# Optimization experiments

Measured on AMD Instinct MI355X. Metric: run time of the kernel, lower is better.

## Reference

```python
import jax, jax.numpy as jnp
import numpy as np

B, T, D = 1, 2048, 1024
H = 16
HD = D // H
K = 4
FF = 4 * D
LAYERS = 24
EPS = 1.1920929e-07  # torch.finfo(float32).eps, RMSNorm default


def setup_inputs() -> dict:
    key = jax.random.key(0)
    ks = jax.random.split(key, 16)
    s = 0.02
    return {
        "x": jax.random.normal(ks[0], (B, T, D), jnp.float32),
        "gamma": jax.random.uniform(ks[1], (D,), jnp.float32),
        "beta": jax.random.normal(ks[2], (D,), jnp.float32) * 0.1,
        "iter_scale": jax.random.uniform(ks[3], (1,), jnp.float32),
        "qkv_bases": jax.random.normal(ks[4], (K, 3 * D, D), jnp.float32) * s,
        "o_bases": jax.random.normal(ks[5], (K, D, D), jnp.float32) * s,
        "gate_bases": jax.random.normal(ks[6], (K, FF, D), jnp.float32) * s,
        "up_bases": jax.random.normal(ks[7], (K, FF, D), jnp.float32) * s,
        "down_bases": jax.random.normal(ks[8], (K, D, FF), jnp.float32) * s,
        "alpha_qkv": jax.random.normal(ks[9], (LAYERS, K), jnp.float32) * 0.1 + jnp.eye(LAYERS, K)[:, :K] * 0.0 + jnp.concatenate([jnp.ones((LAYERS, 1)), jnp.zeros((LAYERS, K - 1))], axis=1),
        "alpha_o": jnp.concatenate([jnp.ones((LAYERS, 1)), jnp.zeros((LAYERS, K - 1))], axis=1) + jax.random.normal(ks[10], (LAYERS, K)) * 0.1,
        "alpha_gate": jnp.concatenate([jnp.ones((LAYERS, 1)), jnp.zeros((LAYERS, K - 1))], axis=1) + jax.random.normal(ks[11], (LAYERS, K)) * 0.1,
        "alpha_up": jnp.concatenate([jnp.ones((LAYERS, 1)), jnp.zeros((LAYERS, K - 1))], axis=1) + jax.random.normal(ks[12], (LAYERS, K)) * 0.1,
        "alpha_down": jnp.concatenate([jnp.ones((LAYERS, 1)), jnp.zeros((LAYERS, K - 1))], axis=1) + jax.random.normal(ks[13], (LAYERS, K)) * 0.1,
        "norm1_w": jnp.ones((D,), jnp.float32),
        "norm2_w": jnp.ones((D,), jnp.float32),
        "layer_idx": 5,
    }


def _rmsnorm(x, w):
    return x * jax.lax.rsqrt(jnp.mean(x * x, axis=-1, keepdims=True) + EPS) * w


def reference(x, gamma, beta, iter_scale, qkv_bases, o_bases, gate_bases, up_bases,
              down_bases, alpha_qkv, alpha_o, alpha_gate, alpha_up, alpha_down,
              norm1_w, norm2_w, layer_idx):
    Bx, Tx, Dx = x.shape
    # --- attention sub-block ---
    h = _rmsnorm(x, norm1_w) * gamma + beta
    W_qkv = jnp.einsum('k,kij->ij', alpha_qkv[layer_idx], qkv_bases)  # [3D, D]
    qkv = jnp.einsum('btd,od->bto', h, W_qkv).reshape(Bx, Tx, 3, H, HD)
    qkv = jnp.transpose(qkv, (2, 0, 3, 1, 4))  # [3, B, H, T, HD]
    q, k, v = qkv[0], qkv[1], qkv[2]
    scores = jnp.einsum('bhqd,bhkd->bhqk', q, k) / jnp.sqrt(jnp.asarray(HD, x.dtype))
    causal = jnp.tril(jnp.ones((Tx, Tx), bool))
    scores = jnp.where(causal, scores, jnp.asarray(-jnp.inf, scores.dtype))
    attn = jax.nn.softmax(scores, axis=-1)
    out = jnp.einsum('bhqk,bhkd->bhqd', attn, v)
    out = jnp.transpose(out, (0, 2, 1, 3)).reshape(Bx, Tx, Dx)
    W_o = jnp.einsum('k,kij->ij', alpha_o[layer_idx], o_bases)
    x_attn = x + jnp.einsum('btd,od->bto', out, W_o)
    # --- SwiGLU FFN sub-block ---
    h2 = _rmsnorm(x_attn, norm2_w) * gamma + beta
    W_g = jnp.einsum('k,kij->ij', alpha_gate[layer_idx], gate_bases)
    W_u = jnp.einsum('k,kij->ij', alpha_up[layer_idx], up_bases)
    W_d = jnp.einsum('k,kij->ij', alpha_down[layer_idx], down_bases)
    gate = jnp.einsum('btd,fd->btf', h2, W_g)
    up = jnp.einsum('btd,fd->btf', h2, W_u)
    ffn_out = jnp.einsum('btf,df->btd', jax.nn.silu(gate) * up, W_d)
    block_out = x_attn + ffn_out
    return x + (block_out - x) * iter_scale
```

## Files before the change

### kernel.cpp

```cpp
#include <hip/hip_runtime.h>
#include <hip/hip_bf16.h>
#include <math.h>

typedef __bf16 bf16;
typedef __bf16 bf16x8 __attribute__((ext_vector_type(8)));
typedef __bf16 bf16x4 __attribute__((ext_vector_type(4)));
typedef float f32x4 __attribute__((ext_vector_type(4)));

#define EPSc 1.1920929e-07f
#define LOG2E 1.44269504f

static __device__ __forceinline__ void glds16(const void* g, void* l) {
  __builtin_amdgcn_global_load_lds((const __attribute__((address_space(1))) void*)g,
                                   (__attribute__((address_space(3))) void*)l, 16, 0, 0);
}

static __device__ __forceinline__ bf16x4 comb4(const float* b0, const float* b1,
                                               const float* b2, const float* b3,
                                               float a0, float a1, float a2, float a3) {
  float4 v0 = *(const float4*)b0, v1 = *(const float4*)b1;
  float4 v2 = *(const float4*)b2, v3 = *(const float4*)b3;
  bf16x4 o;
  o[0] = (bf16)(a0*v0.x + a1*v1.x + a2*v2.x + a3*v3.x);
  o[1] = (bf16)(a0*v0.y + a1*v1.y + a2*v2.y + a3*v3.y);
  o[2] = (bf16)(a0*v0.z + a1*v1.z + a2*v2.z + a3*v3.z);
  o[3] = (bf16)(a0*v0.w + a1*v1.w + a2*v2.w + a3*v3.w);
  return o;
}

__global__ __launch_bounds__(256)
void prep1(const float* __restrict__ qkv_b, const float* __restrict__ a_qkv,
           const float* __restrict__ o_b,   const float* __restrict__ a_o,
           const float* __restrict__ x, const float* __restrict__ n1w,
           const float* __restrict__ gamma, const float* __restrict__ beta,
           const int* __restrict__ lidx,
           bf16* __restrict__ Wqkv, bf16* __restrict__ Wo, bf16* __restrict__ hbuf) {
  const int bid = blockIdx.x, tid = threadIdx.x;
  if (bid < 4096) {
    int li = lidx[0];
    const float* base; const float* al; bf16* out; size_t flat, n;
    if (bid < 3072) { base = qkv_b; al = a_qkv; out = Wqkv; flat = (size_t)bid << 10; n = (size_t)3072*1024; }
    else            { base = o_b;   al = a_o;   out = Wo;   flat = (size_t)(bid-3072) << 10; n = (size_t)1024*1024; }
    float a0 = al[li*4], a1 = al[li*4+1], a2 = al[li*4+2], a3 = al[li*4+3];
    size_t off = flat + tid*4;
    bf16x4 o = comb4(base+off, base+n+off, base+2*n+off, base+3*n+off, a0, a1, a2, a3);
    *(bf16x4*)&out[off] = o;
  } else {
    int row = bid - 4096, t = tid;
    const float4* xr = (const float4*)(x + (size_t)row*1024);
    float4 v = xr[t];
    float ss = v.x*v.x + v.y*v.y + v.z*v.z + v.w*v.w;
    #pragma unroll
    for (int off = 32; off > 0; off >>= 1) ss += __shfl_down(ss, off, 64);
    __shared__ float red[4];
    if ((t & 63) == 0) red[t >> 6] = ss;
    __syncthreads();
    float tot = red[0] + red[1] + red[2] + red[3];
    float r = rsqrtf(tot * (1.0f/1024.0f) + EPSc);
    float4 wv = ((const float4*)n1w)[t];
    float4 gv = ((const float4*)gamma)[t];
    float4 bv = ((const float4*)beta)[t];
    bf16x4 o;
    o[0] = (bf16)(v.x*r*wv.x*gv.x + bv.x);
    o[1] = (bf16)(v.y*r*wv.y*gv.y + bv.y);
    o[2] = (bf16)(v.z*r*wv.z*gv.z + bv.z);
    o[3] = (bf16)(v.w*r*wv.w*gv.w + bv.w);
    *(bf16x4*)&hbuf[(size_t)row*1024 + t*4] = o;
  }
}

__global__ __launch_bounds__(256) void rmsnorm_k(const float* __restrict__ x,
                                                 const float* __restrict__ w,
                                                 const float* __restrict__ gamma,
                                                 const float* __restrict__ beta,
                                                 bf16* __restrict__ out) {
  int row = blockIdx.x, t = threadIdx.x;
  const float4* xr = (const float4*)(x + (size_t)row*1024);
  float4 v = xr[t];
  float ss = v.x*v.x + v.y*v.y + v.z*v.z + v.w*v.w;
  #pragma unroll
  for (int off = 32; off > 0; off >>= 1) ss += __shfl_down(ss, off, 64);
  __shared__ float red[4];
  if ((t & 63) == 0) red[t >> 6] = ss;
  __syncthreads();
  float tot = red[0] + red[1] + red[2] + red[3];
  float r = rsqrtf(tot * (1.0f/1024.0f) + EPSc);
  float4 wv = ((const float4*)w)[t];
  float4 gv = ((const float4*)gamma)[t];
  float4 bv = ((const float4*)beta)[t];
  bf16x4 o;
  o[0] = (bf16)(v.x*r*wv.x*gv.x + bv.x);
  o[1] = (bf16)(v.y*r*wv.y*gv.y + bv.y);
  o[2] = (bf16)(v.z*r*wv.z*gv.z + bv.z);
  o[3] = (bf16)(v.w*r*wv.w*gv.w + bv.w);
  *(bf16x4*)&out[(size_t)row*1024 + t*4] = o;
}

__global__ __launch_bounds__(256)
void transp_v(const bf16* __restrict__ qkvb, bf16* __restrict__ vT) {
  __shared__ bf16 T[64*72];
  const int h = blockIdx.x & 15, tb = blockIdx.x >> 4;
  const int tid = threadIdx.x;
  const int r = tid >> 3, c0 = (tid & 7) << 3;
  bf16x8 v0 = *(const bf16x8*)(qkvb + (size_t)(tb*64 + r)*3072 + 2048 + h*64 + c0);
  bf16x8 v1 = *(const bf16x8*)(qkvb + (size_t)(tb*64 + r + 32)*3072 + 2048 + h*64 + c0);
  #pragma unroll
  for (int e = 0; e < 8; ++e) { T[(c0+e)*72 + r] = v0[e]; T[(c0+e)*72 + r + 32] = v1[e]; }
  __syncthreads();
  bf16x8 o0 = *(const bf16x8*)&T[r*72 + c0];
  bf16x8 o1 = *(const bf16x8*)&T[(r+32)*72 + c0];
  *(bf16x8*)(vT + (size_t)(h*64 + r)*2048 + tb*64 + c0) = o0;
  *(bf16x8*)(vT + (size_t)(h*64 + r + 32)*2048 + tb*64 + c0) = o1;
}

template<int EP, int NTW>
__global__ __launch_bounds__(256)
void gemm_bt(const bf16* __restrict__ A, const bf16* __restrict__ Bw,
             int M, int N, int K, int lda, int ldb, int gx,
             float* __restrict__ outf, bf16* __restrict__ outb,
             const float* __restrict__ auxf, const float* __restrict__ auxf2,
             const float* __restrict__ iscale) {
  constexpr int BN = NTW * 32;
  __shared__ __align__(16) bf16 As[2][128*64];
  __shared__ __align__(16) bf16 Bs[2][BN*64];
  const int nwg = gridDim.x;
  const int orig = blockIdx.x;
  const int wg = (orig & 7) * (nwg >> 3) + (orig >> 3);
  const int tn0 = (wg % gx) * BN, tm0 = (wg / gx) * 128;
  const int tid = threadIdx.x, wave = tid >> 6, lane = tid & 63;
  const int lr = lane & 15, lg = lane >> 4;
  const int wr = wave >> 1, wc = wave & 1;
  f32x4 acc[4][NTW] = {};
  const int rs = lane >> 3;
  const int sc = (((lane & 7) ^ rs) << 3);
  const int x0 = ((lg ^ (lr & 7)) << 3);
  const int x1 = (((4 + lg) ^ (lr & 7)) << 3);

  const bf16* Abase = A + (size_t)tm0 * lda;
  const bf16* Bbase = Bw + (size_t)tn0 * ldb;

  auto stage = [&](bf16* as, bf16* bs, int k0) {
    #pragma unroll
    for (int j = 0; j < 4; ++j) {
      int chunk = wave*4 + j;
      int r = chunk*8 + rs;
      glds16(Abase + (size_t)r*lda + k0 + sc, as + chunk*512 + lane*8);
    }
    #pragma unroll
    for (int j = 0; j < NTW; ++j) {
      int chunk = wave*NTW + j;
      int r = chunk*8 + rs;
      glds16(Bbase + (size_t)r*ldb + k0 + sc, bs + chunk*512 + lane*8);
    }
  };
  auto comp = [&](const bf16* as, const bf16* bs) {
    #pragma unroll
    for (int kk = 0; kk < 2; ++kk) {
      const int x = kk ? x1 : x0;
      bf16x8 av[4], bv[NTW];
      #pragma unroll
      for (int m = 0; m < 4; ++m) av[m] = *(const bf16x8*)&as[(wr*64 + m*16 + lr)*64 + x];
      #pragma unroll
      for (int n = 0; n < NTW; ++n) bv[n] = *(const bf16x8*)&bs[(wc*NTW*16 + n*16 + lr)*64 + x];
      #pragma unroll
      for (int m = 0; m < 4; ++m)
        #pragma unroll
        for (int n = 0; n < NTW; ++n)
          acc[m][n] = __builtin_amdgcn_mfma_f32_16x16x32_bf16(av[m], bv[n], acc[m][n], 0, 0, 0);
    }
  };

  bf16 *a0 = As[0], *a1 = As[1], *b0 = Bs[0], *b1 = Bs[1];
  stage(a0, b0, 0);
  __syncthreads();
  for (int k0 = 64; k0 < K; k0 += 64) {
    stage(a1, b1, k0);
    comp(a0, b0);
    __syncthreads();
    bf16* t;
    t = a0; a0 = a1; a1 = t;
    t = b0; b0 = b1; b1 = t;
  }
  comp(a0, b0);

  float its = 0.f;
  if constexpr (EP == 4) its = iscale[0];
  #pragma unroll
  for (int m = 0; m < 4; ++m)
    #pragma unroll
    for (int n = 0; n < NTW; ++n)
      #pragma unroll
      for (int i = 0; i < 4; ++i) {
        int row = tm0 + wr*64 + m*16 + lg*4 + i;
        int col = tn0 + wc*NTW*16 + n*16 + lr;
        size_t idx = (size_t)row * N + col;
        float v = acc[m][n][i];
        if constexpr (EP == 0) outb[idx] = (bf16)v;
        else if constexpr (EP == 1) outf[idx] = auxf[idx] + v;
        else if constexpr (EP == 4) {
          float xv = auxf[idx], xa = auxf2[idx];
          outf[idx] = xv + (xa + v - xv) * its;
        }
      }
}

__global__ __launch_bounds__(512, 2)
void gemm_gu256(const bf16* __restrict__ A, const bf16* __restrict__ Bw,
                bf16* __restrict__ outb) {
  __shared__ __align__(16) bf16 L[2][2][2][8192];
  const int orig = blockIdx.x;
  const int wg = (orig & 7) * 32 + (orig >> 3);
  const int tn0 = (wg & 31) * 256, tm0 = (wg >> 5) * 256;
  const int tid = threadIdx.x, wave = tid >> 6, lane = tid & 63;
  const int lr = lane & 15, lg = lane >> 4;
  const int wr = wave >> 2, wn = wave & 3;
  const int rs8 = lane >> 3;
  const int gc8 = (((lane & 7) ^ rs8) << 3);
  const int xk0 = ((lg ^ (lr & 7)) << 3);
  const int xk1 = (((4 + lg) ^ (lr & 7)) << 3);
  f32x4 acc[8][4] = {};

  const bf16* Ab = A + (size_t)tm0 * 1024;
  const bf16* Bb = Bw + (size_t)tn0 * 1024;

  auto stage_half = [&](bf16* dst, const bf16* gbase, int half, int k0) {
    #pragma unroll
    for (int l = 0; l < 2; ++l) {
      int r = half*128 + (wave*2 + l)*8 + rs8;
      glds16(gbase + (size_t)r*1024 + k0 + gc8, dst + (wave*2 + l)*512 + lane*8);
    }
  };

  stage_half(&L[0][0][0][0], Ab, 0, 0);
  stage_half(&L[0][0][1][0], Ab, 1, 0);
  stage_half(&L[0][1][0][0], Bb, 0, 0);
  stage_half(&L[0][1][1][0], Bb, 1, 0);
  stage_half(&L[1][1][0][0], Bb, 0, 64);
  stage_half(&L[1][1][1][0], Bb, 1, 64);
  asm volatile("s_waitcnt vmcnt(4)" ::: "memory");
  __builtin_amdgcn_s_barrier();

  for (int t = 0; t < 16; ++t) {
    const int b = t & 1;
    const bf16* ah = &L[b][0][wr][0];
    const bf16* bh = &L[b][1][wn >> 1][0];
    bf16x8 breg[4][2];
    #pragma unroll
    for (int p = 0; p < 4; ++p) {
      if (p == 0) {
        #pragma unroll
        for (int n = 0; n < 4; ++n) {
          int row = (wn & 1)*64 + n*16 + lr;
          breg[n][0] = *(const bf16x8*)&bh[row*64 + xk0];
          breg[n][1] = *(const bf16x8*)&bh[row*64 + xk1];
        }
      }
      bf16x8 av[2][2];
      #pragma unroll
      for (int mi = 0; mi < 2; ++mi) {
        int row = p*32 + mi*16 + lr;
        av[mi][0] = *(const bf16x8*)&ah[row*64 + xk0];
        av[mi][1] = *(const bf16x8*)&ah[row*64 + xk1];
      }
      if (p == 0 && t < 15) stage_half(&L[b^1][0][0][0], Ab, 0, (t+1)*64);
      if (p == 1 && t < 15) stage_half(&L[b^1][0][1][0], Ab, 1, (t+1)*64);
      if (p == 2 && t < 14) stage_half(&L[b][1][0][0], Bb, 0, (t+2)*64);
      if (p == 3 && t < 14) stage_half(&L[b][1][1][0], Bb, 1, (t+2)*64);
      __builtin_amdgcn_s_barrier();
      __builtin_amdgcn_s_setprio(1);
      #pragma unroll
      for (int mi = 0; mi < 2; ++mi)
        #pragma unroll
        for (int n = 0; n < 4; ++n) {
          acc[p*2+mi][n] = __builtin_amdgcn_mfma_f32_16x16x32_bf16(av[mi][0], breg[n][0], acc[p*2+mi][n], 0, 0, 0);
          acc[p*2+mi][n] = __builtin_amdgcn_mfma_f32_16x16x32_bf16(av[mi][1], breg[n][1], acc[p*2+mi][n], 0, 0, 0);
        }
      __builtin_amdgcn_s_setprio(0);
      if (p == 3) {
        if (t >= 14) asm volatile("s_waitcnt vmcnt(0)" ::: "memory");
        else         asm volatile("s_waitcnt vmcnt(4)" ::: "memory");
      }
      __builtin_amdgcn_s_barrier();
    }
  }

  #pragma unroll
  for (int mf = 0; mf < 8; ++mf)
    #pragma unroll
    for (int j = 0; j < 2; ++j)
      #pragma unroll
      for (int i = 0; i < 4; ++i) {
        int row = tm0 + wr*128 + mf*16 + lg*4 + i;
        int col = (tn0 >> 1) + wn*32 + j*16 + lr;
        float g = acc[mf][2*j][i], u = acc[mf][2*j+1][i];
        float s = g / (1.f + __builtin_amdgcn_exp2f(-g * LOG2E));
        outb[(size_t)row * 4096 + col] = (bf16)(s * u);
      }
}

__global__ __launch_bounds__(256)
void attn_merge(const float* __restrict__ oPart, const float* __restrict__ mPart,
                const float* __restrict__ lPart, bf16* __restrict__ out) {
  const int q = blockIdx.x, tid = threadIdx.x;
  const int h = tid >> 4;
  const size_t HQ = (size_t)16 * 2048;
  float mA = mPart[h*2048 + q],      mB = mPart[HQ + h*2048 + q];
  float lA = lPart[h*2048 + q],      lB = lPart[HQ + h*2048 + q];
  float fm = fmaxf(mA, mB);
  float eA = __builtin_amdgcn_exp2f(mA - fm);
  float eB = __builtin_amdgcn_exp2f(mB - fm);
  float inv = 1.f / (lA*eA + lB*eB);
  const size_t QD = (size_t)2048 * 1024;
  size_t idx = (size_t)q*1024 + tid*4;
  float4 oA = *(const float4*)&oPart[idx];
  float4 oB = *(const float4*)&oPart[QD + idx];
  bf16x4 o;
  o[0] = (bf16)((oA.x*eA + oB.x*eB) * inv);
  o[1] = (bf16)((oA.y*eA + oB.y*eB) * inv);
  o[2] = (bf16)((oA.z*eA + oB.z*eB) * inv);
  o[3] = (bf16)((oA.w*eA + oB.w*eB) * inv);
  *(bf16x4*)&out[idx] = o;
}

__global__ __launch_bounds__(256)
void attn_mega(const bf16* __restrict__ qkv, const bf16* __restrict__ vT,
               const float* __restrict__ gate_b, const float* __restrict__ up_b,
               const float* __restrict__ down_b,
               const float* __restrict__ a_gate, const float* __restrict__ a_up,
               const float* __restrict__ a_down, const int* __restrict__ lidx,
               bf16* __restrict__ Wgu, bf16* __restrict__ Wd,
               float* __restrict__ oPart, float* __restrict__ mPart,
               float* __restrict__ lPart) {
  __shared__ __align__(16) bf16 Ks[2][64*64];
  __shared__ __align__(16) bf16 VT[2][64*64];
  __shared__ __align__(16) bf16 Ps[4][2][16*68];
  const int bid = blockIdx.x;
  const int tid = threadIdx.x;

  if (bid < 256) {
    const int cb = bid;
    int li = lidx[0];
    float g0 = a_gate[li*4], g1 = a_gate[li*4+1], g2 = a_gate[li*4+2], g3 = a_gate[li*4+3];
    float u0 = a_up[li*4],   u1 = a_up[li*4+1],   u2 = a_up[li*4+2],   u3 = a_up[li*4+3];
    float d0 = a_down[li*4], d1 = a_down[li*4+1], d2 = a_down[li*4+2], d3 = a_down[li*4+3];
    const size_t PS = (size_t)4096 * 1024;
    for (int it = 0; it < 48; ++it) {
      int chunk = it * 256 + cb;
      if (chunk < 8192) {
        int r = chunk, w = r & 31;
        int f = ((r >> 5) << 4) + (w & 15);
        const float* base = (w < 16) ? gate_b : up_b;
        float a0 = (w < 16) ? g0 : u0, a1 = (w < 16) ? g1 : u1;
        float a2 = (w < 16) ? g2 : u2, a3 = (w < 16) ? g3 : u3;
        size_t src = (size_t)f*1024 + tid*4;
        bf16x4 o = comb4(base+src, base+PS+src, base+2*PS+src, base+3*PS+src, a0, a1, a2, a3);
        *(bf16x4*)&Wgu[((size_t)r << 10) + tid*4] = o;
      } else {
        size_t off = ((size_t)(chunk - 8192) << 10) + tid*4;
        bf16x4 o = comb4(down_b+off, down_b+PS+off, down_b+2*PS+off, down_b+3*PS+off, d0, d1, d2, d3);
        *(bf16x4*)&Wd[off] = o;
      }
    }
    return;
  }

  const int a = bid - 256;
  const int sp = a >> 8;
  const int rem = a & 255;
  const int qb = 15 - (rem >> 4);
  const int h = rem & 15;
  const int wave = tid >> 6, lane = tid & 63;
  const int lr = lane & 15, lg = lane >> 4;
  const int q0 = qb * 128;
  const int qw = q0 + wave * 32;
  const int t0 = sp * (qb + 1), t1 = t0 + (qb + 1);

  bf16x8 qf[2][2];
  #pragma unroll
  for (int qt = 0; qt < 2; ++qt) {
    const bf16* qrow = qkv + (size_t)(qw + qt*16 + lr)*3072 + h*64;
    qf[qt][0] = *(const bf16x8*)(qrow + lg*8);
    qf[qt][1] = *(const bf16x8*)(qrow + 32 + lg*8);
  }
  f32x4 o[2][4] = {};
  float mrow[2], lrow[2];
  mrow[0] = mrow[1] = -__builtin_inff();
  lrow[0] = lrow[1] = 0.f;
  const int xsrc = (lane & 48) | (lg << 2);

  const int rs = tid >> 3;
  const int cs8 = ((tid & 7) ^ (rs & 7)) << 3;
  const bf16* kb = qkv + 1024 + h*64 + cs8;
  const bf16* vb = vT + (size_t)(h*64)*2048 + cs8;
  const int xk0 = ((lg ^ (lr & 7)) << 3);
  const int xk1 = (((4 + lg) ^ (lr & 7)) << 3);

  auto stage = [&](int buf, int kv0) {
    glds16(kb + (size_t)(kv0 + rs)*3072,      &Ks[buf][tid*8]);
    glds16(kb + (size_t)(kv0 + rs + 32)*3072, &Ks[buf][2048 + tid*8]);
    glds16(vb + (size_t)rs*2048 + kv0,        &VT[buf][tid*8]);
    glds16(vb + (size_t)(rs + 32)*2048 + kv0, &VT[buf][2048 + tid*8]);
  };

  stage(0, t0 * 64);
  __syncthreads();
  int cur = 0;

  const float C = 0.125f * LOG2E;

  for (int t = t0; t < t1; ++t) {
    const int kv0 = t * 64;
    if (t < t1-1) stage(cur ^ 1, kv0 + 64);

    f32x4 s[2][4] = {};
    __builtin_amdgcn_s_setprio(1);
    #pragma unroll
    for (int n = 0; n < 4; ++n) {
      bf16x8 k0f = *(const bf16x8*)&Ks[cur][(n*16 + lr)*64 + xk0];
      bf16x8 k1f = *(const bf16x8*)&Ks[cur][(n*16 + lr)*64 + xk1];
      #pragma unroll
      for (int qt = 0; qt < 2; ++qt) {
        s[qt][n] = __builtin_amdgcn_mfma_f32_16x16x32_bf16(k0f, qf[qt][0], s[qt][n], 0, 0, 0);
        s[qt][n] = __builtin_amdgcn_mfma_f32_16x16x32_bf16(k1f, qf[qt][1], s[qt][n], 0, 0, 0);
      }
    }
    __builtin_amdgcn_s_setprio(0);

    if (kv0 + 63 > qw) {
      #pragma unroll
      for (int qt = 0; qt < 2; ++qt) {
        const int qv = qw + qt*16 + lr;
        #pragma unroll
        for (int n = 0; n < 4; ++n)
          #pragma unroll
          for (int i = 0; i < 4; ++i)
            if (kv0 + n*16 + lg*4 + i > qv) s[qt][n][i] = -__builtin_inff();
      }
    }

    float pmn[2];
    #pragma unroll
    for (int qt = 0; qt < 2; ++qt) {
      f32x4 u0 = s[qt][0], u1 = s[qt][1];
      #pragma unroll
      for (int i = 0; i < 4; ++i) { u0[i] = fmaxf(u0[i], s[qt][2][i]); u1[i] = fmaxf(u1[i], s[qt][3][i]); }
      float a0 = fmaxf(u0[0], u0[1]), a1 = fmaxf(u0[2], u0[3]);
      float b0 = fmaxf(u1[0], u1[1]), b1 = fmaxf(u1[2], u1[3]);
      float mnew = fmaxf(fmaxf(a0, a1), fmaxf(b0, b1));
      mnew = fmaxf(mnew, __shfl_xor(mnew, 16, 64));
      mnew = fmaxf(mnew, __shfl_xor(mnew, 32, 64));
      pmn[qt] = mnew * C;
    }
    bool grow = (pmn[0] > mrow[0] + 8.f) || (pmn[1] > mrow[1] + 8.f);
    if (__any(grow)) {
      #pragma unroll
      for (int qt = 0; qt < 2; ++qt) {
        float mt = fmaxf(mrow[qt], pmn[qt]);
        float fc = __builtin_amdgcn_exp2f(mrow[qt] - mt);
        mrow[qt] = mt;
        lrow[qt] *= fc;
        #pragma unroll
        for (int i = 0; i < 4; ++i) {
          float fci = __shfl(fc, xsrc + i, 64);
          #pragma unroll
          for (int nd = 0; nd < 4; ++nd) o[qt][nd][i] *= fci;
        }
      }
    }
    #pragma unroll
    for (int qt = 0; qt < 2; ++qt) {
      float mref = fmaxf(mrow[qt], -3e38f);
      float rsum = 0.f;
      #pragma unroll
      for (int n = 0; n < 4; ++n) {
        bf16x4 p4;
        #pragma unroll
        for (int i = 0; i < 4; ++i) {
          float e = __builtin_amdgcn_exp2f(__builtin_fmaf(s[qt][n][i], C, -mref));
          rsum += e;
          p4[i] = (bf16)e;
        }
        *(bf16x4*)&Ps[wave][qt][lr*68 + n*16 + lg*4] = p4;
      }
      rsum += __shfl_xor(rsum, 16, 64);
      rsum += __shfl_xor(rsum, 32, 64);
      lrow[qt] += rsum;
    }
    asm volatile("s_waitcnt lgkmcnt(0)" ::: "memory");

    #pragma unroll
    for (int kk = 0; kk < 2; ++kk) {
      const int xk = kk ? xk1 : xk0;
      bf16x8 pf0 = *(const bf16x8*)&Ps[wave][0][lr*68 + kk*32 + lg*8];
      bf16x8 pf1 = *(const bf16x8*)&Ps[wave][1][lr*68 + kk*32 + lg*8];
      __builtin_amdgcn_s_setprio(1);
      #pragma unroll
      for (int nd = 0; nd < 4; ++nd) {
        bf16x8 vf = *(const bf16x8*)&VT[cur][(nd*16 + lr)*64 + xk];
        o[0][nd] = __builtin_amdgcn_mfma_f32_16x16x32_bf16(pf0, vf, o[0][nd], 0, 0, 0);
        o[1][nd] = __builtin_amdgcn_mfma_f32_16x16x32_bf16(pf1, vf, o[1][nd], 0, 0, 0);
      }
      __builtin_amdgcn_s_setprio(0);
    }
    if (t < t1-1) {
      __syncthreads();
      cur ^= 1;
    }
  }

  float* oP = oPart + (size_t)sp * 2048 * 1024;
  #pragma unroll
  for (int qt = 0; qt < 2; ++qt) {
    #pragma unroll
    for (int i = 0; i < 4; ++i) {
      size_t row = (size_t)(qw + qt*16 + lg*4 + i)*1024 + h*64;
      #pragma unroll
      for (int nd = 0; nd < 4; ++nd)
        oP[row + nd*16 + lr] = o[qt][nd][i];
    }
    if (lane < 16) {
      size_t si = (size_t)sp * 16 * 2048 + (size_t)h * 2048 + qw + qt*16 + lr;
      mPart[si] = mrow[qt];
      lPart[si] = lrow[qt];
    }
  }
}

extern "C" void kernel_launch(void* const* d_in, const int* in_sizes, int n_in,
                              void* d_out, int out_size, void* d_ws, size_t ws_size,
                              hipStream_t stream) {
  const float* x        = (const float*)d_in[0];
  const float* gamma    = (const float*)d_in[1];
  const float* beta     = (const float*)d_in[2];
  const float* iscale   = (const float*)d_in[3];
  const float* qkv_b    = (const float*)d_in[4];
  const float* o_b      = (const float*)d_in[5];
  const float* gate_b   = (const float*)d_in[6];
  const float* up_b     = (const float*)d_in[7];
  const float* down_b   = (const float*)d_in[8];
  const float* a_qkv    = (const float*)d_in[9];
  const float* a_o      = (const float*)d_in[10];
  const float* a_gate   = (const float*)d_in[11];
  const float* a_up     = (const float*)d_in[12];
  const float* a_down   = (const float*)d_in[13];
  const float* n1w      = (const float*)d_in[14];
  const float* n2w      = (const float*)d_in[15];
  const int*   lidx     = (const int*)d_in[16];

  char* p = (char*)d_ws;
  auto alloc = [&](size_t bytes) { char* r = p; p += (bytes + 255) & ~(size_t)255; return r; };
  bf16*  Wqkv = (bf16*)alloc((size_t)3072*1024*2);
  bf16*  Wo   = (bf16*)alloc((size_t)1024*1024*2);
  bf16*  Wgu  = (bf16*)alloc((size_t)8192*1024*2);
  bf16*  Wd   = (bf16*)alloc((size_t)1024*4096*2);
  bf16*  hbuf = (bf16*)alloc((size_t)2048*1024*2);
  bf16*  qkvb = (bf16*)alloc((size_t)2048*3072*2);
  bf16*  vTb  = (bf16*)alloc((size_t)1024*2048*2);
  bf16*  attn = (bf16*)alloc((size_t)2048*1024*2);
  float* xat  = (float*)alloc((size_t)2048*1024*4);
  bf16*  h2   = (bf16*)alloc((size_t)2048*1024*2);
  bf16*  act  = (bf16*)alloc((size_t)2048*4096*2);
  float* oPart = (float*)alloc((size_t)2*2048*1024*4);
  float* mPart = (float*)alloc((size_t)2*16*2048*4);
  float* lPart = (float*)alloc((size_t)2*16*2048*4);
  float* out  = (float*)d_out;

  prep1<<<6144, 256, 0, stream>>>(qkv_b, a_qkv, o_b, a_o, x, n1w, gamma, beta, lidx,
                                  Wqkv, Wo, hbuf);
  gemm_bt<0,4><<<24*16, 256, 0, stream>>>(hbuf, Wqkv, 2048, 3072, 1024, 1024, 1024, 24,
                                          nullptr, qkvb, nullptr, nullptr, nullptr);
  transp_v<<<512, 256, 0, stream>>>(qkvb, vTb);
  attn_mega<<<768, 256, 0, stream>>>(qkvb, vTb, gate_b, up_b, down_b,
                                     a_gate, a_up, a_down, lidx, Wgu, Wd,
                                     oPart, mPart, lPart);
  attn_merge<<<2048, 256, 0, stream>>>(oPart, mPart, lPart, attn);
  gemm_bt<1,2><<<16*16, 256, 0, stream>>>(attn, Wo, 2048, 1024, 1024, 1024, 1024, 16,
                                          xat, nullptr, x, nullptr, nullptr);
  rmsnorm_k<<<2048, 256, 0, stream>>>(xat, n2w, gamma, beta, h2);
  gemm_gu256<<<256, 512, 0, stream>>>(h2, Wgu, act);
  gemm_bt<4,2><<<16*16, 256, 0, stream>>>(act, Wd, 2048, 1024, 4096, 4096, 4096, 16,
                                          out, nullptr, x, xat, iscale);
}
```

Before: 194.6 us.

## Co-schedule FFN weight combine with QKV GEMM and register-pipeline attention KV loads

New measurement: 211.8 us. +8.8%, slower.

```diff
diff --git a/kernel.cpp b/kernel.cpp
--- a/kernel.cpp
+++ b/kernel.cpp
@@ -18,13 +18,15 @@
 static __device__ __forceinline__ bf16x4 comb4(const float* b0, const float* b1,
                                                const float* b2, const float* b3,
                                                float a0, float a1, float a2, float a3) {
-  float4 v0 = *(const float4*)b0, v1 = *(const float4*)b1;
-  float4 v2 = *(const float4*)b2, v3 = *(const float4*)b3;
+  f32x4 v0 = __builtin_nontemporal_load((const f32x4*)b0);
+  f32x4 v1 = __builtin_nontemporal_load((const f32x4*)b1);
+  f32x4 v2 = __builtin_nontemporal_load((const f32x4*)b2);
+  f32x4 v3 = __builtin_nontemporal_load((const f32x4*)b3);
   bf16x4 o;
-  o[0] = (bf16)(a0*v0.x + a1*v1.x + a2*v2.x + a3*v3.x);
-  o[1] = (bf16)(a0*v0.y + a1*v1.y + a2*v2.y + a3*v3.y);
-  o[2] = (bf16)(a0*v0.z + a1*v1.z + a2*v2.z + a3*v3.z);
-  o[3] = (bf16)(a0*v0.w + a1*v1.w + a2*v2.w + a3*v3.w);
+  o[0] = (bf16)(a0*v0[0] + a1*v1[0] + a2*v2[0] + a3*v3[0]);
+  o[1] = (bf16)(a0*v0[1] + a1*v1[1] + a2*v2[1] + a3*v3[1]);
+  o[2] = (bf16)(a0*v0[2] + a1*v1[2] + a2*v2[2] + a3*v3[2]);
+  o[3] = (bf16)(a0*v0[3] + a1*v1[3] + a2*v2[3] + a3*v3[3]);
   return o;
 }
 
@@ -113,6 +115,111 @@
   *(bf16x8*)(vT + (size_t)(h*64 + r + 32)*2048 + tb*64 + c0) = o1;
 }
 
+__global__ __launch_bounds__(256)
+void qkv_mega(const bf16* __restrict__ A, const bf16* __restrict__ Bw,
+              bf16* __restrict__ outb,
+              const float* __restrict__ gate_b, const float* __restrict__ up_b,
+              const float* __restrict__ down_b,
+              const float* __restrict__ a_gate, const float* __restrict__ a_up,
+              const float* __restrict__ a_down, const int* __restrict__ lidx,
+              bf16* __restrict__ Wgu, bf16* __restrict__ Wd) {
+  __shared__ __align__(16) bf16 As[2][128*64];
+  __shared__ __align__(16) bf16 Bs[2][128*64];
+  const int bid = blockIdx.x, tid = threadIdx.x;
+
+  if (bid < 256) {
+    const int cb = bid;
+    int li = lidx[0];
+    float g0 = a_gate[li*4], g1 = a_gate[li*4+1], g2 = a_gate[li*4+2], g3 = a_gate[li*4+3];
+    float u0 = a_up[li*4],   u1 = a_up[li*4+1],   u2 = a_up[li*4+2],   u3 = a_up[li*4+3];
+    float d0 = a_down[li*4], d1 = a_down[li*4+1], d2 = a_down[li*4+2], d3 = a_down[li*4+3];
+    const size_t PS = (size_t)4096 * 1024;
+    for (int it = 0; it < 48; ++it) {
+      int chunk = it * 256 + cb;
+      if (chunk < 8192) {
+        int r = chunk, w = r & 31;
+        int f = ((r >> 5) << 4) + (w & 15);
+        const float* base = (w < 16) ? gate_b : up_b;
+        float a0 = (w < 16) ? g0 : u0, a1 = (w < 16) ? g1 : u1;
+        float a2 = (w < 16) ? g2 : u2, a3 = (w < 16) ? g3 : u3;
+        size_t src = (size_t)f*1024 + tid*4;
+        bf16x4 o = comb4(base+src, base+PS+src, base+2*PS+src, base+3*PS+src, a0, a1, a2, a3);
+        *(bf16x4*)&Wgu[((size_t)r << 10) + tid*4] = o;
+      } else {
+        size_t off = ((size_t)(chunk - 8192) << 10) + tid*4;
+        bf16x4 o = comb4(down_b+off, down_b+PS+off, down_b+2*PS+off, down_b+3*PS+off, d0, d1, d2, d3);
+        *(bf16x4*)&Wd[off] = o;
+      }
+    }
+    return;
+  }
+
+  const int orig = bid - 256;
+  const int wg = (orig & 7) * 48 + (orig >> 3);
+  const int tn0 = (wg % 24) * 128, tm0 = (wg / 24) * 128;
+  const int wave = tid >> 6, lane = tid & 63;
+  const int lr = lane & 15, lg = lane >> 4;
+  const int wr = wave >> 1, wc = wave & 1;
+  f32x4 acc[4][4] = {};
+  const int rs = lane >> 3;
+  const int sc = (((lane & 7) ^ rs) << 3);
+  const int x0 = ((lg ^ (lr & 7)) << 3);
+  const int x1 = (((4 + lg) ^ (lr & 7)) << 3);
+
+  const bf16* Abase = A + (size_t)tm0 * 1024;
+  const bf16* Bbase = Bw + (size_t)tn0 * 1024;
+
+  auto stage = [&](bf16* as, bf16* bs, int k0) {
+    #pragma unroll
+    for (int j = 0; j < 4; ++j) {
+      int chunk = wave*4 + j;
+      int r = chunk*8 + rs;
+      glds16(Abase + (size_t)r*1024 + k0 + sc, as + chunk*512 + lane*8);
+      glds16(Bbase + (size_t)r*1024 + k0 + sc, bs + chunk*512 + lane*8);
+    }
+  };
+  auto comp = [&](const bf16* as, const bf16* bs) {
+    #pragma unroll
+    for (int kk = 0; kk < 2; ++kk) {
+      const int x = kk ? x1 : x0;
+      bf16x8 av[4], bv[4];
+      #pragma unroll
+      for (int m = 0; m < 4; ++m) av[m] = *(const bf16x8*)&as[(wr*64 + m*16 + lr)*64 + x];
+      #pragma unroll
+      for (int n = 0; n < 4; ++n) bv[n] = *(const bf16x8*)&bs[(wc*64 + n*16 + lr)*64 + x];
+      #pragma unroll
+      for (int m = 0; m < 4; ++m)
+        #pragma unroll
+        for (int n = 0; n < 4; ++n)
+          acc[m][n] = __builtin_amdgcn_mfma_f32_16x16x32_bf16(av[m], bv[n], acc[m][n], 0, 0, 0);
+    }
+  };
+
+  bf16 *a0 = As[0], *a1 = As[1], *b0 = Bs[0], *b1 = Bs[1];
+  stage(a0, b0, 0);
+  __syncthreads();
+  for (int k0 = 64; k0 < 1024; k0 += 64) {
+    stage(a1, b1, k0);
+    comp(a0, b0);
+    __syncthreads();
+    bf16* t;
+    t = a0; a0 = a1; a1 = t;
+    t = b0; b0 = b1; b1 = t;
+  }
+  comp(a0, b0);
+
+  #pragma unroll
+  for (int m = 0; m < 4; ++m)
+    #pragma unroll
+    for (int n = 0; n < 4; ++n)
+      #pragma unroll
+      for (int i = 0; i < 4; ++i) {
+        int row = tm0 + wr*64 + m*16 + lg*4 + i;
+        int col = tn0 + wc*64 + n*16 + lr;
+        outb[(size_t)row * 3072 + col] = (bf16)acc[m][n][i];
+      }
+}
+
 template<int EP, int NTW>
 __global__ __launch_bounds__(256)
 void gemm_bt(const bf16* __restrict__ A, const bf16* __restrict__ Bw,
@@ -323,48 +430,14 @@
 }
 
 __global__ __launch_bounds__(256)
-void attn_mega(const bf16* __restrict__ qkv, const bf16* __restrict__ vT,
-               const float* __restrict__ gate_b, const float* __restrict__ up_b,
-               const float* __restrict__ down_b,
-               const float* __restrict__ a_gate, const float* __restrict__ a_up,
-               const float* __restrict__ a_down, const int* __restrict__ lidx,
-               bf16* __restrict__ Wgu, bf16* __restrict__ Wd,
-               float* __restrict__ oPart, float* __restrict__ mPart,
-               float* __restrict__ lPart) {
+void attn_k(const bf16* __restrict__ qkv, const bf16* __restrict__ vT,
+            float* __restrict__ oPart, float* __restrict__ mPart,
+            float* __restrict__ lPart) {
   __shared__ __align__(16) bf16 Ks[2][64*64];
   __shared__ __align__(16) bf16 VT[2][64*64];
   __shared__ __align__(16) bf16 Ps[4][2][16*68];
-  const int bid = blockIdx.x;
+  const int a = blockIdx.x;
   const int tid = threadIdx.x;
-
-  if (bid < 256) {
-    const int cb = bid;
-    int li = lidx[0];
-    float g0 = a_gate[li*4], g1 = a_gate[li*4+1], g2 = a_gate[li*4+2], g3 = a_gate[li*4+3];
-    float u0 = a_up[li*4],   u1 = a_up[li*4+1],   u2 = a_up[li*4+2],   u3 = a_up[li*4+3];
-    float d0 = a_down[li*4], d1 = a_down[li*4+1], d2 = a_down[li*4+2], d3 = a_down[li*4+3];
-    const size_t PS = (size_t)4096 * 1024;
-    for (int it = 0; it < 48; ++it) {
-      int chunk = it * 256 + cb;
-      if (chunk < 8192) {
-        int r = chunk, w = r & 31;
-        int f = ((r >> 5) << 4) + (w & 15);
-        const float* base = (w < 16) ? gate_b : up_b;
-        float a0 = (w < 16) ? g0 : u0, a1 = (w < 16) ? g1 : u1;
-        float a2 = (w < 16) ? g2 : u2, a3 = (w < 16) ? g3 : u3;
-        size_t src = (size_t)f*1024 + tid*4;
-        bf16x4 o = comb4(base+src, base+PS+src, base+2*PS+src, base+3*PS+src, a0, a1, a2, a3);
-        *(bf16x4*)&Wgu[((size_t)r << 10) + tid*4] = o;
-      } else {
-        size_t off = ((size_t)(chunk - 8192) << 10) + tid*4;
-        bf16x4 o = comb4(down_b+off, down_b+PS+off, down_b+2*PS+off, down_b+3*PS+off, d0, d1, d2, d3);
-        *(bf16x4*)&Wd[off] = o;
-      }
-    }
-    return;
-  }
-
-  const int a = bid - 256;
   const int sp = a >> 8;
   const int rem = a & 255;
   const int qb = 15 - (rem >> 4);
@@ -395,23 +468,33 @@
   const int xk0 = ((lg ^ (lr & 7)) << 3);
   const int xk1 = (((4 + lg) ^ (lr & 7)) << 3);
 
-  auto stage = [&](int buf, int kv0) {
-    glds16(kb + (size_t)(kv0 + rs)*3072,      &Ks[buf][tid*8]);
-    glds16(kb + (size_t)(kv0 + rs + 32)*3072, &Ks[buf][2048 + tid*8]);
-    glds16(vb + (size_t)rs*2048 + kv0,        &VT[buf][tid*8]);
-    glds16(vb + (size_t)(rs + 32)*2048 + kv0, &VT[buf][2048 + tid*8]);
-  };
-
-  stage(0, t0 * 64);
-  __syncthreads();
+  bf16x8 krA0, krA1, vrA0, vrA1, krB0, krB1, vrB0, vrB1;
+  auto loadA = [&](int kv0) {
+    krA0 = *(const bf16x8*)(kb + (size_t)(kv0 + rs)*3072);
+    krA1 = *(const bf16x8*)(kb + (size_t)(kv0 + rs + 32)*3072);
+    vrA0 = *(const bf16x8*)(vb + (size_t)rs*2048 + kv0);
+    vrA1 = *(const bf16x8*)(vb + (size_t)(rs + 32)*2048 + kv0);
+  };
+  auto loadB = [&](int kv0) {
+    krB0 = *(const bf16x8*)(kb + (size_t)(kv0 + rs)*3072);
+    krB1 = *(const bf16x8*)(kb + (size_t)(kv0 + rs + 32)*3072);
+    vrB0 = *(const bf16x8*)(vb + (size_t)rs*2048 + kv0);
+    vrB1 = *(const bf16x8*)(vb + (size_t)(rs + 32)*2048 + kv0);
+  };
+  auto writeA = [&](int buf) {
+    *(bf16x8*)&Ks[buf][tid*8] = krA0;  *(bf16x8*)&Ks[buf][2048 + tid*8] = krA1;
+    *(bf16x8*)&VT[buf][tid*8] = vrA0;  *(bf16x8*)&VT[buf][2048 + tid*8] = vrA1;
+  };
+  auto writeB = [&](int buf) {
+    *(bf16x8*)&Ks[buf][tid*8] = krB0;  *(bf16x8*)&Ks[buf][2048 + tid*8] = krB1;
+    *(bf16x8*)&VT[buf][tid*8] = vrB0;  *(bf16x8*)&VT[buf][2048 + tid*8] = vrB1;
+  };
+
+  const float C = 0.125f * LOG2E;
   int cur = 0;
 
-  const float C = 0.125f * LOG2E;
-
-  for (int t = t0; t < t1; ++t) {
+  auto compute = [&](int t) {
     const int kv0 = t * 64;
-    if (t < t1-1) stage(cur ^ 1, kv0 + 64);
-
     f32x4 s[2][4] = {};
     __builtin_amdgcn_s_setprio(1);
     #pragma unroll
@@ -502,10 +585,35 @@
       }
       __builtin_amdgcn_s_setprio(0);
     }
-    if (t < t1-1) {
-      __syncthreads();
+  };
+
+  loadA(t0 * 64);
+  writeA(0);
+  if (t0 + 1 < t1) loadA((t0 + 1) * 64);
+  asm volatile("s_waitcnt lgkmcnt(0)" ::: "memory");
+  __builtin_amdgcn_s_barrier();
+
+  int t = t0;
+  while (t < t1) {
+    if (t + 2 < t1) loadB((t + 2) * 64);
+    compute(t);
+    if (t + 1 < t1) {
+      writeA(cur ^ 1);
+      asm volatile("s_waitcnt lgkmcnt(0)" ::: "memory");
+      __builtin_amdgcn_s_barrier();
       cur ^= 1;
     }
+    ++t;
+    if (t >= t1) break;
+    if (t + 2 < t1) loadA((t + 2) * 64);
+    compute(t);
+    if (t + 1 < t1) {
+      writeB(cur ^ 1);
+      asm volatile("s_waitcnt lgkmcnt(0)" ::: "memory");
+      __builtin_amdgcn_s_barrier();
+      cur ^= 1;
+    }
+    ++t;
   }
 
   float* oP = oPart + (size_t)sp * 2048 * 1024;
@@ -567,12 +675,10 @@
 
   prep1<<<6144, 256, 0, stream>>>(qkv_b, a_qkv, o_b, a_o, x, n1w, gamma, beta, lidx,
                                   Wqkv, Wo, hbuf);
-  gemm_bt<0,4><<<24*16, 256, 0, stream>>>(hbuf, Wqkv, 2048, 3072, 1024, 1024, 1024, 24,
-                                          nullptr, qkvb, nullptr, nullptr, nullptr);
+  qkv_mega<<<640, 256, 0, stream>>>(hbuf, Wqkv, qkvb, gate_b, up_b, down_b,
+                                    a_gate, a_up, a_down, lidx, Wgu, Wd);
   transp_v<<<512, 256, 0, stream>>>(qkvb, vTb);
-  attn_mega<<<768, 256, 0, stream>>>(qkvb, vTb, gate_b, up_b, down_b,
-                                     a_gate, a_up, a_down, lidx, Wgu, Wd,
-                                     oPart, mPart, lPart);
+  attn_k<<<512, 256, 0, stream>>>(qkvb, vTb, oPart, mPart, lPart);
   attn_merge<<<2048, 256, 0, stream>>>(oPart, mPart, lPart, attn);
   gemm_bt<1,2><<<16*16, 256, 0, stream>>>(attn, Wo, 2048, 1024, 1024, 1024, 1024, 16,
                                           xat, nullptr, x, nullptr, nullptr);
```
